# Kernel tuning notes

Measured on AMD Instinct MI355X. Metric: run time of the kernel, lower is better.

## Reference

```python
import jax, jax.numpy as jnp
import numpy as np

VOCAB = 23
PAD_IDX = 21
SOS_IDX = 22
LATENT = 128
COND = 16
HID = 1024
EMB = 512
MAX_LEN = 64
B = 4096


def setup_inputs() -> dict:
    key = jax.random.key(0)
    ks = jax.random.split(key, 12)
    s = lambda *d: 1.0 / np.sqrt(d[-1])
    inp = {
        "z": jax.random.normal(ks[0], (B, LATENT), jnp.float32),
        "cond": jax.random.normal(ks[1], (B, COND), jnp.float32),
        "emb_table": jax.random.normal(ks[2], (VOCAB, EMB), jnp.float32),
        "W_lh": jax.random.uniform(ks[3], (HID, LATENT + COND), jnp.float32, -s(LATENT + COND), s(LATENT + COND)),
        "b_lh": jax.random.uniform(ks[4], (HID,), jnp.float32, -s(LATENT + COND), s(LATENT + COND)),
        "W_ih": jax.random.uniform(ks[5], (4 * HID, EMB), jnp.float32, -s(HID), s(HID)),
        "W_hh": jax.random.uniform(ks[6], (4 * HID, HID), jnp.float32, -s(HID), s(HID)),
        "b_ih": jax.random.uniform(ks[7], (4 * HID,), jnp.float32, -s(HID), s(HID)),
        "b_hh": jax.random.uniform(ks[8], (4 * HID,), jnp.float32, -s(HID), s(HID)),
        "W_out": jax.random.uniform(ks[9], (VOCAB, HID), jnp.float32, -s(HID), s(HID)),
        "b_out": jax.random.uniform(ks[10], (VOCAB,), jnp.float32, -s(HID), s(HID)),
    }
    return inp


def reference(z, cond, emb_table, W_lh, b_lh, W_ih, W_hh, b_ih, b_hh, W_out, b_out):
    # padding_idx row of the embedding is zero (and non-trainable in torch)
    E = emb_table.at[PAD_IDX].set(0.0)
    # initial hidden from latent+cond; initial cell is zeros
    h0 = jnp.concatenate([z, cond], axis=1) @ W_lh.T + b_lh          # [B, H]
    c0 = jnp.zeros_like(h0)
    x0 = E[jnp.full((z.shape[0],), SOS_IDX, dtype=jnp.int32)]        # [B, E]
    bias = b_ih + b_hh

    def step(carry, _):
        h, c, x = carry
        gates = x @ W_ih.T + h @ W_hh.T + bias                        # [B, 4H]
        i, f, g, o = jnp.split(gates, 4, axis=1)
        i = jax.nn.sigmoid(i)
        f = jax.nn.sigmoid(f)
        g = jnp.tanh(g)
        o = jax.nn.sigmoid(o)
        c = f * c + i * g
        h = o * jnp.tanh(c)
        logits = h @ W_out.T + b_out                                  # [B, V]
        nxt = jnp.argmax(logits, axis=1)                              # greedy token
        x = E[nxt]
        return (h, c, x), logits

    _, logits_t = jax.lax.scan(step, (h0, c0, x0), None, length=MAX_LEN)  # [T, B, V]
    return jnp.transpose(logits_t, (1, 0, 2))                         # [B, T, V]
```

## Files before the change

kernel.cpp:

```cpp
#include <hip/hip_runtime.h>

#define NB 4096
#define NH 1024
#define NE 512
#define NV 23
#define NT 64
#define NL 144
#define PADV 21
#define SOSV 22

typedef unsigned short u16;
typedef __attribute__((ext_vector_type(4))) float f32x4;
typedef __attribute__((ext_vector_type(8))) __bf16 bf16x8;
typedef __attribute__((ext_vector_type(8))) unsigned short u16x8;

__device__ __forceinline__ u16 f2bf(float x) {
  unsigned u = __float_as_uint(x);
  u += 0x7FFFu + ((u >> 16) & 1u);
  return (u16)(u >> 16);
}
__device__ __forceinline__ float bf2f(u16 h) {
  return __uint_as_float(((unsigned)h) << 16);
}

__device__ __forceinline__ size_t hidx(int m, int j) {
  return ((size_t)(((m >> 8) * 32 + (j >> 5)) * 4 + ((j >> 3) & 3)) * 2048)
         + (size_t)((m & 255) * 8) + (j & 7);
}

__global__ void prep_kernel(const float* __restrict__ Whh, u16* __restrict__ Whi,
                            u16* __restrict__ Wlo, float* __restrict__ c,
                            int* __restrict__ tok) {
  int i = blockIdx.x * 256 + threadIdx.x;
  float wv = Whh[i];
  u16 hi = f2bf(wv);
  u16 lo = f2bf(wv - bf2f(hi));
  const int nw = i >> 10, k = i & 1023;
  const int g = nw >> 10, jcol = nw & 1023;
  const int jt = jcol >> 6, jl = jcol & 63;
  const int row = ((jl >> 4) << 6) + (g << 4) + (jl & 15);
  const size_t oi = ((size_t)((jt * 32 + (k >> 5)) * 4 + ((k >> 3) & 3)) * 2048)
                    + (size_t)(row * 8) + (k & 7);
  Whi[oi] = hi;
  Wlo[oi] = lo;
  c[i] = 0.0f;
  if (i < NB) tok[i] = SOSV;
}

__global__ void exw_kernel(const float* __restrict__ emb, const float* __restrict__ Wih,
                           const float* __restrict__ bih, const float* __restrict__ bhh,
                           float* __restrict__ ExW) {
  __shared__ float Es[NE];
  const int v = blockIdx.y;
  const int n = blockIdx.x * 256 + threadIdx.x;
  for (int k = threadIdx.x; k < NE; k += 256)
    Es[k] = (v == PADV) ? 0.0f : emb[v * NE + k];
  __syncthreads();
  float s = bih[n] + bhh[n];
  const float* wr = Wih + (long)n * NE;
  for (int k = 0; k < NE; ++k) s = fmaf(Es[k], wr[k], s);
  ExW[v * (4 * NH) + n] = s;
}

__global__ void h0_kernel(const float* __restrict__ z, const float* __restrict__ cnd,
                          const float* __restrict__ Wlh, const float* __restrict__ blh,
                          u16* __restrict__ hhi, u16* __restrict__ hlo) {
  __shared__ float zc[8][NL];
  const int b0 = blockIdx.y * 8;
  const int j = blockIdx.x * 256 + threadIdx.x;
  for (int idx = threadIdx.x; idx < 8 * NL; idx += 256) {
    int bi = idx / NL, k = idx % NL;
    zc[bi][k] = (k < 128) ? z[(long)(b0 + bi) * 128 + k]
                          : cnd[(long)(b0 + bi) * 16 + (k - 128)];
  }
  __syncthreads();
  float acc[8];
  const float bj = blh[j];
#pragma unroll
  for (int bi = 0; bi < 8; ++bi) acc[bi] = bj;
  const float* wr = Wlh + (long)j * NL;
  for (int k = 0; k < NL; ++k) {
    float wv = wr[k];
#pragma unroll
    for (int bi = 0; bi < 8; ++bi) acc[bi] = fmaf(wv, zc[bi][k], acc[bi]);
  }
#pragma unroll
  for (int bi = 0; bi < 8; ++bi) {
    size_t idx = hidx(b0 + bi, j);
    u16 hi = f2bf(acc[bi]);
    hhi[idx] = hi;
    hlo[idx] = f2bf(acc[bi] - bf2f(hi));
  }
}

__device__ __forceinline__ void stage1(const u16* __restrict__ src, u16* dst, int i) {
  __builtin_amdgcn_global_load_lds(
      (const __attribute__((address_space(1))) void*)(src + i * 512),
      (__attribute__((address_space(3))) void*)(dst + i * 512), 16, 0, 0);
}

__global__ __launch_bounds__(512, 2)
void gates_cell_kernel(const u16* __restrict__ Whi, const u16* __restrict__ Wlo,
                       const u16* __restrict__ hhi_in, const u16* __restrict__ hlo_in,
                       const float* __restrict__ ExW, const int* __restrict__ tok,
                       float* __restrict__ c, u16* __restrict__ hhi_out,
                       u16* __restrict__ hlo_out) {
  __shared__ u16 lds[65536];

  const int bid = blockIdx.x;
  const int swz = (bid & 7) * 32 + (bid >> 3);
  const int jt = swz >> 4;
  const int mt = swz & 15;
  const int m0 = mt << 8;
  const int j0 = jt << 6;

  const int tid = threadIdx.x;
  const int w = tid >> 6, l = tid & 63;
  const int wm = w >> 1, wn = w & 1;
  const int q = l >> 4, rL = l & 15;

  const int mat = w >> 1, hf = w & 1;
  const u16* simg = (mat == 0) ? hhi_in : (mat == 1) ? hlo_in : (mat == 2) ? Whi : Wlo;
  const size_t sbase = ((mat < 2) ? ((size_t)mt * 262144) : ((size_t)jt * 262144))
                       + (size_t)hf * 4096 + (size_t)l * 8;
  const u16* sit = simg + sbase;
  u16* dwave = (u16*)lds + mat * 16384 + hf * 4096;

  int tkv[16];
#pragma unroll
  for (int mi = 0; mi < 4; ++mi)
#pragma unroll
    for (int r = 0; r < 4; ++r)
      tkv[mi * 4 + r] = tok[m0 + wm * 64 + mi * 16 + q * 4 + r];

  f32x4 acc[4][8];
#pragma unroll
  for (int mi = 0; mi < 4; ++mi)
#pragma unroll
    for (int ni = 0; ni < 8; ++ni) acc[mi][ni] = (f32x4){0.f, 0.f, 0.f, 0.f};

  const int qoff = q * 2048 + rL * 8;

#pragma unroll
  for (int i = 0; i < 8; ++i) stage1(sit, dwave, i);
  asm volatile("s_waitcnt vmcnt(0)" ::: "memory");
  __builtin_amdgcn_s_barrier();
  __builtin_amdgcn_sched_barrier(0);

  int buf = 0;
  for (int ks = 0; ks < 32; ++ks) {
    const u16* ab = lds + buf * 8192 + qoff + wm * 512;
    const u16* bb = lds + 32768 + buf * 8192 + qoff + wn * 1024;
    const u16* snext = sit + (size_t)(ks + 1) * 8192;
    u16* dnext = dwave + (buf ^ 1) * 8192;
    bf16x8 ah[4], al[4];

#pragma unroll
    for (int ph = 0; ph < 4; ++ph) {
      if (ph == 0) {
#pragma unroll
        for (int mi = 0; mi < 4; ++mi) {
          ah[mi] = *reinterpret_cast<const bf16x8*>(ab + mi * 128);
          al[mi] = *reinterpret_cast<const bf16x8*>(ab + 16384 + mi * 128);
        }
      }
      bf16x8 bh0 = *reinterpret_cast<const bf16x8*>(bb + (2 * ph + 0) * 128);
      bf16x8 bl0 = *reinterpret_cast<const bf16x8*>(bb + 16384 + (2 * ph + 0) * 128);
      bf16x8 bh1 = *reinterpret_cast<const bf16x8*>(bb + (2 * ph + 1) * 128);
      bf16x8 bl1 = *reinterpret_cast<const bf16x8*>(bb + 16384 + (2 * ph + 1) * 128);
      if (ks < 31) {
        if (ph == 0) { stage1(snext, dnext, 0); stage1(snext, dnext, 1); stage1(snext, dnext, 2); }
        if (ph == 1) { stage1(snext, dnext, 3); stage1(snext, dnext, 4); stage1(snext, dnext, 5); }
        if (ph == 2) { stage1(snext, dnext, 6); stage1(snext, dnext, 7); }
      }
      __builtin_amdgcn_sched_barrier(0);
      __builtin_amdgcn_s_barrier();
      __builtin_amdgcn_sched_barrier(0);
      __builtin_amdgcn_s_setprio(1);
#pragma unroll
      for (int mi = 0; mi < 4; ++mi)
        acc[mi][2 * ph + 0] = __builtin_amdgcn_mfma_f32_16x16x32_bf16(ah[mi], bh0, acc[mi][2 * ph + 0], 0, 0, 0);
#pragma unroll
      for (int mi = 0; mi < 4; ++mi)
        acc[mi][2 * ph + 0] = __builtin_amdgcn_mfma_f32_16x16x32_bf16(ah[mi], bl0, acc[mi][2 * ph + 0], 0, 0, 0);
#pragma unroll
      for (int mi = 0; mi < 4; ++mi)
        acc[mi][2 * ph + 0] = __builtin_amdgcn_mfma_f32_16x16x32_bf16(al[mi], bh0, acc[mi][2 * ph + 0], 0, 0, 0);
#pragma unroll
      for (int mi = 0; mi < 4; ++mi)
        acc[mi][2 * ph + 1] = __builtin_amdgcn_mfma_f32_16x16x32_bf16(ah[mi], bh1, acc[mi][2 * ph + 1], 0, 0, 0);
#pragma unroll
      for (int mi = 0; mi < 4; ++mi)
        acc[mi][2 * ph + 1] = __builtin_amdgcn_mfma_f32_16x16x32_bf16(ah[mi], bl1, acc[mi][2 * ph + 1], 0, 0, 0);
#pragma unroll
      for (int mi = 0; mi < 4; ++mi)
        acc[mi][2 * ph + 1] = __builtin_amdgcn_mfma_f32_16x16x32_bf16(al[mi], bh1, acc[mi][2 * ph + 1], 0, 0, 0);
      __builtin_amdgcn_s_setprio(0);
      __builtin_amdgcn_sched_barrier(0);
    }

    if (ks < 31) {
      asm volatile("s_waitcnt vmcnt(0)" ::: "memory");
      __builtin_amdgcn_s_barrier();
      __builtin_amdgcn_sched_barrier(0);
    }
    buf ^= 1;
  }

#pragma unroll
  for (int mi = 0; mi < 4; ++mi) {
#pragma unroll
    for (int r = 0; r < 4; ++r) {
      const int m = m0 + wm * 64 + mi * 16 + q * 4 + r;
      const float* exr = ExW + (size_t)tkv[mi * 4 + r] * 4096;
#pragma unroll
      for (int jh = 0; jh < 2; ++jh) {
        const int j = j0 + (wn * 2 + jh) * 16 + rL;
        const float gi = acc[mi][jh * 4 + 0][r] + exr[j];
        const float gf = acc[mi][jh * 4 + 1][r] + exr[NH + j];
        const float gg = acc[mi][jh * 4 + 2][r] + exr[2 * NH + j];
        const float go = acc[mi][jh * 4 + 3][r] + exr[3 * NH + j];
        const float i_ = 1.0f / (1.0f + expf(-gi));
        const float f_ = 1.0f / (1.0f + expf(-gf));
        const float g_ = tanhf(gg);
        const float o_ = 1.0f / (1.0f + expf(-go));
        const size_t cidx = (size_t)m * NH + j;
        const float cn = f_ * c[cidx] + i_ * g_;
        c[cidx] = cn;
        const float hn = o_ * tanhf(cn);
        const u16 hi = f2bf(hn);
        const size_t oidx = hidx(m, j);
        hhi_out[oidx] = hi;
        hlo_out[oidx] = f2bf(hn - bf2f(hi));
      }
    }
  }
}

__global__ __launch_bounds__(256)
void logits_kernel(const u16* __restrict__ hhi, const u16* __restrict__ hlo,
                   const float* __restrict__ Wout, const float* __restrict__ bout,
                   float* __restrict__ out, int* __restrict__ tok, int t) {
  __shared__ float hs[8][NH];
  __shared__ float part[8][24][8];
  __shared__ float lg[8][24];
  const int b0 = blockIdx.x * 8;
  const int tid = threadIdx.x;
  for (int ci = tid; ci < 1024; ci += 256) {
    const int bi = ci >> 7, cj = ci & 127;
    const int m = b0 + bi;
    const int ks = cj >> 2, qq = cj & 3;
    const size_t base = ((size_t)(((m >> 8) * 32 + ks) * 4 + qq) * 2048)
                        + (size_t)((m & 255) * 8);
    const u16x8 vh = *reinterpret_cast<const u16x8*>(hhi + base);
    const u16x8 vl = *reinterpret_cast<const u16x8*>(hlo + base);
    const int kb = ks * 32 + qq * 8;
#pragma unroll
    for (int e = 0; e < 8; ++e) hs[bi][kb + e] = bf2f(vh[e]) + bf2f(vl[e]);
  }
  __syncthreads();
  const int v = tid & 31, kc = tid >> 5;
  if (v < NV) {
    float s[8];
#pragma unroll
    for (int bi = 0; bi < 8; ++bi) s[bi] = 0.f;
    const float* wr = Wout + (long)v * NH + kc * 128;
    const int kb = kc * 128;
    for (int k = 0; k < 128; ++k) {
      float wv = wr[k];
#pragma unroll
      for (int bi = 0; bi < 8; ++bi) s[bi] = fmaf(wv, hs[bi][kb + k], s[bi]);
    }
#pragma unroll
    for (int bi = 0; bi < 8; ++bi) part[kc][v][bi] = s[bi];
  }
  __syncthreads();
  if (tid < NV * 8) {
    const int vv = tid >> 3, bi = tid & 7;
    float s = bout[vv];
#pragma unroll
    for (int k = 0; k < 8; ++k) s += part[k][vv][bi];
    lg[bi][vv] = s;
    out[((long)(b0 + bi) * NT + t) * NV + vv] = s;
  }
  __syncthreads();
  if (tid < 8) {
    float best = lg[tid][0];
    int bv = 0;
    for (int vv = 1; vv < NV; ++vv) {
      float x = lg[tid][vv];
      if (x > best) { best = x; bv = vv; }
    }
    tok[b0 + tid] = bv;
  }
}

extern "C" void kernel_launch(void* const* d_in, const int* in_sizes, int n_in,
                              void* d_out, int out_size, void* d_ws, size_t ws_size,
                              hipStream_t stream) {
  const float* z    = (const float*)d_in[0];
  const float* cnd  = (const float*)d_in[1];
  const float* emb  = (const float*)d_in[2];
  const float* Wlh  = (const float*)d_in[3];
  const float* blh  = (const float*)d_in[4];
  const float* Wih  = (const float*)d_in[5];
  const float* Whh  = (const float*)d_in[6];
  const float* bih  = (const float*)d_in[7];
  const float* bhh  = (const float*)d_in[8];
  const float* Wout = (const float*)d_in[9];
  const float* bout = (const float*)d_in[10];
  float* out = (float*)d_out;

  char* ws = (char*)d_ws;
  size_t off = 0;
  auto alloc = [&](size_t bytes) -> void* {
    off = (off + 255) & ~(size_t)255;
    void* p = ws + off;
    off += bytes;
    return p;
  };
  u16* Whi = (u16*)alloc((size_t)4 * NH * NH * 2);
  u16* Wlo = (u16*)alloc((size_t)4 * NH * NH * 2);
  float* ExW = (float*)alloc((size_t)NV * 4 * NH * 4);
  u16* hhi0 = (u16*)alloc((size_t)NB * NH * 2);
  u16* hhi1 = (u16*)alloc((size_t)NB * NH * 2);
  u16* hlo0 = (u16*)alloc((size_t)NB * NH * 2);
  u16* hlo1 = (u16*)alloc((size_t)NB * NH * 2);
  float* cbuf = (float*)alloc((size_t)NB * NH * 4);
  int* tokb = (int*)alloc((size_t)NB * 4);
  u16* hhi[2] = {hhi0, hhi1};
  u16* hlo[2] = {hlo0, hlo1};

  prep_kernel<<<dim3((4 * NH * NH) / 256), dim3(256), 0, stream>>>(Whh, Whi, Wlo, cbuf, tokb);
  exw_kernel<<<dim3((4 * NH) / 256, NV), dim3(256), 0, stream>>>(emb, Wih, bih, bhh, ExW);
  h0_kernel<<<dim3(NH / 256, NB / 8), dim3(256), 0, stream>>>(z, cnd, Wlh, blh, hhi[0], hlo[0]);

  int p = 0;
  for (int t = 0; t < NT; ++t) {
    gates_cell_kernel<<<dim3(256), dim3(512), 0, stream>>>(
        Whi, Wlo, hhi[p], hlo[p], ExW, tokb, cbuf, hhi[p ^ 1], hlo[p ^ 1]);
    logits_kernel<<<dim3(NB / 8), dim3(256), 0, stream>>>(
        hhi[p ^ 1], hlo[p ^ 1], Wout, bout, out, tokb, t);
    p ^= 1;
  }
}
```

Before: 6.330 ms.

## Retile LSTM gate GEMM to 128-row blocks with register-loaded hidden operand

Restructures the recurrent gate GEMM so each 256-thread block handles 128 batch rows by 256 gate columns, launching 512 blocks instead of 256. The hidden-state operand is now loaded straight from global memory into registers with a double-buffered prefetch. Only the hi/lo weight tiles are staged through LDS, which halves the LDS footprint. The weight layout in prep is changed to a simpler gate-major row order to match. The aim is better occupancy and less LDS traffic, at the cost of direct global A loads that may add latency and using plain __syncthreads instead of the tuned barrier and priority scheduling.

```diff
diff --git a/kernel.cpp b/kernel.cpp
--- a/kernel.cpp
+++ b/kernel.cpp
@@ -38,7 +38,7 @@
   const int nw = i >> 10, k = i & 1023;
   const int g = nw >> 10, jcol = nw & 1023;
   const int jt = jcol >> 6, jl = jcol & 63;
-  const int row = ((jl >> 4) << 6) + (g << 4) + (jl & 15);
+  const int row = g * 64 + jl;
   const size_t oi = ((size_t)((jt * 32 + (k >> 5)) * 4 + ((k >> 3) & 3)) * 2048)
                     + (size_t)(row * 8) + (k & 7);
   Whi[oi] = hi;
@@ -93,25 +93,25 @@
   }
 }
 
-__device__ __forceinline__ void stage1(const u16* __restrict__ src, u16* dst, int i) {
+__device__ __forceinline__ void gll(const u16* src, u16* dst) {
   __builtin_amdgcn_global_load_lds(
-      (const __attribute__((address_space(1))) void*)(src + i * 512),
-      (__attribute__((address_space(3))) void*)(dst + i * 512), 16, 0, 0);
-}
-
-__global__ __launch_bounds__(512, 2)
+      (const __attribute__((address_space(1))) void*)src,
+      (__attribute__((address_space(3))) void*)dst, 16, 0, 0);
+}
+
+__global__ __launch_bounds__(256, 2)
 void gates_cell_kernel(const u16* __restrict__ Whi, const u16* __restrict__ Wlo,
                        const u16* __restrict__ hhi_in, const u16* __restrict__ hlo_in,
                        const float* __restrict__ ExW, const int* __restrict__ tok,
                        float* __restrict__ c, u16* __restrict__ hhi_out,
                        u16* __restrict__ hlo_out) {
-  __shared__ u16 lds[65536];
+  __shared__ u16 lds[32768];
 
   const int bid = blockIdx.x;
-  const int swz = (bid & 7) * 32 + (bid >> 3);
-  const int jt = swz >> 4;
-  const int mt = swz & 15;
-  const int m0 = mt << 8;
+  const int swz = (bid & 7) * 64 + (bid >> 3);
+  const int jt = swz >> 5;
+  const int bm = swz & 31;
+  const int m0 = bm << 7;
   const int j0 = jt << 6;
 
   const int tid = threadIdx.x;
@@ -119,92 +119,72 @@
   const int wm = w >> 1, wn = w & 1;
   const int q = l >> 4, rL = l & 15;
 
-  const int mat = w >> 1, hf = w & 1;
-  const u16* simg = (mat == 0) ? hhi_in : (mat == 1) ? hlo_in : (mat == 2) ? Whi : Wlo;
-  const size_t sbase = ((mat < 2) ? ((size_t)mt * 262144) : ((size_t)jt * 262144))
-                       + (size_t)hf * 4096 + (size_t)l * 8;
-  const u16* sit = simg + sbase;
-  u16* dwave = (u16*)lds + mat * 16384 + hf * 4096;
-
-  int tkv[16];
+  const int smat = w >> 1, shalf = w & 1;
+  const u16* simg = smat ? Wlo : Whi;
+  const size_t sB = (size_t)jt * 262144 + (size_t)shalf * 4096 + (size_t)l * 8;
+  u16* sdst0 = (u16*)lds + smat * 8192 + shalf * 4096 + l * 8;
+
+  const int slab = bm >> 1;
+  const int arow0 = ((bm & 1) << 7) + wm * 64 + rL;
+  const size_t aBase = ((size_t)slab * 128 + q) * 2048 + (size_t)arow0 * 8;
+
+  f32x4 acc[4][8];
 #pragma unroll
   for (int mi = 0; mi < 4; ++mi)
 #pragma unroll
-    for (int r = 0; r < 4; ++r)
-      tkv[mi * 4 + r] = tok[m0 + wm * 64 + mi * 16 + q * 4 + r];
-
-  f32x4 acc[4][8];
-#pragma unroll
-  for (int mi = 0; mi < 4; ++mi)
-#pragma unroll
     for (int ni = 0; ni < 8; ++ni) acc[mi][ni] = (f32x4){0.f, 0.f, 0.f, 0.f};
 
-  const int qoff = q * 2048 + rL * 8;
-
-#pragma unroll
-  for (int i = 0; i < 8; ++i) stage1(sit, dwave, i);
-  asm volatile("s_waitcnt vmcnt(0)" ::: "memory");
-  __builtin_amdgcn_s_barrier();
-  __builtin_amdgcn_sched_barrier(0);
-
-  int buf = 0;
-  for (int ks = 0; ks < 32; ++ks) {
-    const u16* ab = lds + buf * 8192 + qoff + wm * 512;
-    const u16* bb = lds + 32768 + buf * 8192 + qoff + wn * 1024;
-    const u16* snext = sit + (size_t)(ks + 1) * 8192;
-    u16* dnext = dwave + (buf ^ 1) * 8192;
-    bf16x8 ah[4], al[4];
-
-#pragma unroll
-    for (int ph = 0; ph < 4; ++ph) {
-      if (ph == 0) {
-#pragma unroll
-        for (int mi = 0; mi < 4; ++mi) {
-          ah[mi] = *reinterpret_cast<const bf16x8*>(ab + mi * 128);
-          al[mi] = *reinterpret_cast<const bf16x8*>(ab + 16384 + mi * 128);
-        }
+  bf16x8 A0h[4], A0l[4], A1h[4], A1l[4];
+
+#pragma unroll
+  for (int i = 0; i < 8; ++i) gll(simg + sB + i * 512, sdst0 + i * 512);
+#pragma unroll
+  for (int mi = 0; mi < 4; ++mi) {
+    A0h[mi] = *reinterpret_cast<const bf16x8*>(hhi_in + aBase + mi * 128);
+    A0l[mi] = *reinterpret_cast<const bf16x8*>(hlo_in + aBase + mi * 128);
+  }
+  __syncthreads();
+
+  auto body = [&](int ks, int buf, bf16x8* aCh, bf16x8* aCl,
+                  bf16x8* aNh, bf16x8* aNl) {
+    if (ks < 31) {
+      const u16* src = simg + sB + (size_t)(ks + 1) * 8192;
+      u16* dst = sdst0 + (buf ^ 1) * 16384;
+#pragma unroll
+      for (int i = 0; i < 8; ++i) gll(src + i * 512, dst + i * 512);
+      const size_t ao = aBase + (size_t)(ks + 1) * 8192;
+#pragma unroll
+      for (int mi = 0; mi < 4; ++mi) {
+        aNh[mi] = *reinterpret_cast<const bf16x8*>(hhi_in + ao + mi * 128);
+        aNl[mi] = *reinterpret_cast<const bf16x8*>(hlo_in + ao + mi * 128);
       }
-      bf16x8 bh0 = *reinterpret_cast<const bf16x8*>(bb + (2 * ph + 0) * 128);
-      bf16x8 bl0 = *reinterpret_cast<const bf16x8*>(bb + 16384 + (2 * ph + 0) * 128);
-      bf16x8 bh1 = *reinterpret_cast<const bf16x8*>(bb + (2 * ph + 1) * 128);
-      bf16x8 bl1 = *reinterpret_cast<const bf16x8*>(bb + 16384 + (2 * ph + 1) * 128);
-      if (ks < 31) {
-        if (ph == 0) { stage1(snext, dnext, 0); stage1(snext, dnext, 1); stage1(snext, dnext, 2); }
-        if (ph == 1) { stage1(snext, dnext, 3); stage1(snext, dnext, 4); stage1(snext, dnext, 5); }
-        if (ph == 2) { stage1(snext, dnext, 6); stage1(snext, dnext, 7); }
+    }
+    const u16* bb = lds + buf * 16384;
+#pragma unroll
+    for (int ni = 0; ni < 2; ++ni) {
+#pragma unroll
+      for (int g = 0; g < 4; ++g) {
+        const int ro = q * 2048 + (g * 64 + wn * 32 + ni * 16 + rL) * 8;
+        const bf16x8 bh = *reinterpret_cast<const bf16x8*>(bb + ro);
+        const bf16x8 bl = *reinterpret_cast<const bf16x8*>(bb + 8192 + ro);
+        const int ai = g * 2 + ni;
+#pragma unroll
+        for (int mi = 0; mi < 4; ++mi)
+          acc[mi][ai] = __builtin_amdgcn_mfma_f32_16x16x32_bf16(aCh[mi], bh, acc[mi][ai], 0, 0, 0);
+#pragma unroll
+        for (int mi = 0; mi < 4; ++mi)
+          acc[mi][ai] = __builtin_amdgcn_mfma_f32_16x16x32_bf16(aCh[mi], bl, acc[mi][ai], 0, 0, 0);
+#pragma unroll
+        for (int mi = 0; mi < 4; ++mi)
+          acc[mi][ai] = __builtin_amdgcn_mfma_f32_16x16x32_bf16(aCl[mi], bh, acc[mi][ai], 0, 0, 0);
       }
-      __builtin_amdgcn_sched_barrier(0);
-      __builtin_amdgcn_s_barrier();
-      __builtin_amdgcn_sched_barrier(0);
-      __builtin_amdgcn_s_setprio(1);
-#pragma unroll
-      for (int mi = 0; mi < 4; ++mi)
-        acc[mi][2 * ph + 0] = __builtin_amdgcn_mfma_f32_16x16x32_bf16(ah[mi], bh0, acc[mi][2 * ph + 0], 0, 0, 0);
-#pragma unroll
-      for (int mi = 0; mi < 4; ++mi)
-        acc[mi][2 * ph + 0] = __builtin_amdgcn_mfma_f32_16x16x32_bf16(ah[mi], bl0, acc[mi][2 * ph + 0], 0, 0, 0);
-#pragma unroll
-      for (int mi = 0; mi < 4; ++mi)
-        acc[mi][2 * ph + 0] = __builtin_amdgcn_mfma_f32_16x16x32_bf16(al[mi], bh0, acc[mi][2 * ph + 0], 0, 0, 0);
-#pragma unroll
-      for (int mi = 0; mi < 4; ++mi)
-        acc[mi][2 * ph + 1] = __builtin_amdgcn_mfma_f32_16x16x32_bf16(ah[mi], bh1, acc[mi][2 * ph + 1], 0, 0, 0);
-#pragma unroll
-      for (int mi = 0; mi < 4; ++mi)
-        acc[mi][2 * ph + 1] = __builtin_amdgcn_mfma_f32_16x16x32_bf16(ah[mi], bl1, acc[mi][2 * ph + 1], 0, 0, 0);
-#pragma unroll
-      for (int mi = 0; mi < 4; ++mi)
-        acc[mi][2 * ph + 1] = __builtin_amdgcn_mfma_f32_16x16x32_bf16(al[mi], bh1, acc[mi][2 * ph + 1], 0, 0, 0);
-      __builtin_amdgcn_s_setprio(0);
-      __builtin_amdgcn_sched_barrier(0);
-    }
-
-    if (ks < 31) {
-      asm volatile("s_waitcnt vmcnt(0)" ::: "memory");
-      __builtin_amdgcn_s_barrier();
-      __builtin_amdgcn_sched_barrier(0);
-    }
-    buf ^= 1;
+    }
+    __syncthreads();
+  };
+
+  for (int ks2 = 0; ks2 < 32; ks2 += 2) {
+    body(ks2, 0, A0h, A0l, A1h, A1l);
+    body(ks2 + 1, 1, A1h, A1l, A0h, A0l);
   }
 
 #pragma unroll
@@ -212,14 +192,15 @@
 #pragma unroll
     for (int r = 0; r < 4; ++r) {
       const int m = m0 + wm * 64 + mi * 16 + q * 4 + r;
-      const float* exr = ExW + (size_t)tkv[mi * 4 + r] * 4096;
-#pragma unroll
-      for (int jh = 0; jh < 2; ++jh) {
-        const int j = j0 + (wn * 2 + jh) * 16 + rL;
-        const float gi = acc[mi][jh * 4 + 0][r] + exr[j];
-        const float gf = acc[mi][jh * 4 + 1][r] + exr[NH + j];
-        const float gg = acc[mi][jh * 4 + 2][r] + exr[2 * NH + j];
-        const float go = acc[mi][jh * 4 + 3][r] + exr[3 * NH + j];
+      const int tk = tok[m];
+      const float* exr = ExW + (size_t)tk * 4096;
+#pragma unroll
+      for (int ni = 0; ni < 2; ++ni) {
+        const int j = j0 + wn * 32 + ni * 16 + rL;
+        const float gi = acc[mi][0 * 2 + ni][r] + exr[j];
+        const float gf = acc[mi][1 * 2 + ni][r] + exr[NH + j];
+        const float gg = acc[mi][2 * 2 + ni][r] + exr[2 * NH + j];
+        const float go = acc[mi][3 * 2 + ni][r] + exr[3 * NH + j];
         const float i_ = 1.0f / (1.0f + expf(-gi));
         const float f_ = 1.0f / (1.0f + expf(-gf));
         const float g_ = tanhf(gg);
@@ -337,7 +318,7 @@
 
   int p = 0;
   for (int t = 0; t < NT; ++t) {
-    gates_cell_kernel<<<dim3(256), dim3(512), 0, stream>>>(
+    gates_cell_kernel<<<dim3(512), dim3(256), 0, stream>>>(
         Whi, Wlo, hhi[p], hlo[p], ExW, tokb, cbuf, hhi[p ^ 1], hlo[p ^ 1]);
     logits_kernel<<<dim3(NB / 8), dim3(256), 0, stream>>>(
         hhi[p ^ 1], hlo[p ^ 1], Wout, bout, out, tokb, t);
```

Measured after the change: 6.871 ms. 8.5% more time.
